# Kernel tuning notes

Hardware: AMD Instinct MI355X
Metric: run time of the kernel (lower is better)

The kernel has to match this reference:

```python
import jax, jax.numpy as jnp
import numpy as np

NUM_HEADS = 16
N_QUBITS = 8  # both attention d_k and FFN qubit count
LN_EPS = 1e-5


def setup_inputs() -> dict:
    key = jax.random.key(0)
    ks = jax.random.split(key, 8)
    B, S, E, F = 8, 4096, 128, 2048
    return {
        "x": jax.random.normal(ks[0], (B, S, E), dtype=jnp.float32),
        "theta_attn": jax.random.normal(ks[1], (N_QUBITS,), dtype=jnp.float32),
        "phi_ffn": jax.random.normal(ks[2], (N_QUBITS,), dtype=jnp.float32),
        "w1": jax.random.normal(ks[3], (F, N_QUBITS), dtype=jnp.float32) * (1.0 / np.sqrt(N_QUBITS)),
        "b1": jax.random.normal(ks[4], (F,), dtype=jnp.float32) * 0.01,
        "w2": jax.random.normal(ks[5], (E, F), dtype=jnp.float32) * (1.0 / np.sqrt(F)),
        "b2": jax.random.normal(ks[6], (E,), dtype=jnp.float32) * 0.01,
        "gamma1": jnp.ones((E,), dtype=jnp.float32),
        "beta1": jnp.zeros((E,), dtype=jnp.float32),
        "gamma2": jnp.ones((E,), dtype=jnp.float32),
        "beta2": jnp.zeros((E,), dtype=jnp.float32),
    }


def _layernorm(y, g, b):
    m = jnp.mean(y, axis=-1, keepdims=True)
    v = jnp.var(y, axis=-1, keepdims=True)
    return (y - m) * jax.lax.rsqrt(v + LN_EPS) * g + b


def _quantum_attn(x, theta):
    # RX(x_k)RX(theta_k) per wire -> per-wire <Z>=cos(x_k+theta_k); CNOT chain + ring
    # maps Z_j -> Z_0..Z_j (j>=1) and Z_0 -> Z_0..Z_{n-1} (Heisenberg picture),
    # so outputs are cumulative products of cosines within each head.
    B, S, E = x.shape
    a = x.reshape(B, S, NUM_HEADS, N_QUBITS) + theta  # (B,S,H,8)
    cp = jnp.cumprod(jnp.cos(a), axis=-1)
    out = jnp.concatenate([cp[..., -1:], cp[..., 1:]], axis=-1)  # wire0 gets full product
    return out.reshape(B, S, E)


def _quantum_ffn(x, phi):
    # RY(phi_j)RX(x_j)|0> -> <Z_j> = cos(phi_j)*cos(x_j); encoder only reads first N_QUBITS feats
    return jnp.cos(phi) * jnp.cos(x[..., :N_QUBITS])  # (B,S,8)


def reference(x, theta_attn, phi_ffn, w1, b1, w2, b2, gamma1, beta1, gamma2, beta2):
    attn = _quantum_attn(x, theta_attn)
    x1 = _layernorm(x + attn, gamma1, beta1)  # dropout is identity in eval
    q = _quantum_ffn(x1, phi_ffn)
    h = jax.nn.relu(jnp.einsum('bsq,fq->bsf', q, w1) + b1)
    ffn = jnp.einsum('bsf,ef->bse', h, w2) + b2
    return _layernorm(x1 + ffn, gamma2, beta2)
```

## Files before the change

kernel.cpp:

```cpp
#include <hip/hip_runtime.h>
#include <hip/hip_bf16.h>

typedef __attribute__((ext_vector_type(8))) short short8;
typedef __attribute__((ext_vector_type(4))) float f32x4;
typedef __attribute__((ext_vector_type(4))) int int4v;

#define LN_EPS 1e-5f

__device__ __forceinline__ unsigned short bf16rn(float f) {
    unsigned int u = __builtin_bit_cast(unsigned int, f);
    u = u + 0x7fffu + ((u >> 16) & 1u);
    return (unsigned short)(u >> 16);
}

__device__ __forceinline__ unsigned cvt_pk(float lo, float hi) {
    unsigned r;
    asm("v_cvt_pk_bf16_f32 %0, %1, %2" : "=v"(r) : "v"(lo), "v"(hi));
    return r;
}

__global__ __launch_bounds__(256) void k_prep(const float* __restrict__ w2,
                                              const float* __restrict__ w1,
                                              const float* __restrict__ b1,
                                              unsigned short* __restrict__ w2b,
                                              unsigned short* __restrict__ w1p) {
    const int bid = blockIdx.x;
    if (bid < 256) {
        int i = (bid * 256 + threadIdx.x) * 4;
        float4 v = *(const float4*)(w2 + i);
        ushort4 r;
        r.x = bf16rn(v.x); r.y = bf16rn(v.y); r.z = bf16rn(v.z); r.w = bf16rn(v.w);
        *(ushort4*)(w2b + i) = r;
    } else {
        int f = (bid - 256) * 256 + threadIdx.x;
        float4 wa = *(const float4*)(w1 + (size_t)f * 8);
        float4 wb = *(const float4*)(w1 + (size_t)f * 8 + 4);
        short8 r0, r1;
        r0[0] = (short)bf16rn(wa.x); r0[1] = (short)bf16rn(wa.y);
        r0[2] = (short)bf16rn(wa.z); r0[3] = (short)bf16rn(wa.w);
        r0[4] = (short)bf16rn(wb.x); r0[5] = (short)bf16rn(wb.y);
        r0[6] = (short)bf16rn(wb.z); r0[7] = (short)bf16rn(wb.w);
        r1 = short8{0, 0, 0, 0, 0, 0, 0, 0};
        r1[0] = (short)bf16rn(b1[f]);
        short8 z = short8{0, 0, 0, 0, 0, 0, 0, 0};
        unsigned short* row = w1p + (size_t)f * 32;
        *(short8*)(row) = r0;
        *(short8*)(row + 8) = r1;
        *(short8*)(row + 16) = z;
        *(short8*)(row + 24) = z;
    }
}

__global__ __launch_bounds__(256) void k_pre(const float* __restrict__ x,
                                             const float* __restrict__ theta,
                                             const float* __restrict__ phi,
                                             const float* __restrict__ gamma1,
                                             const float* __restrict__ beta1,
                                             float* __restrict__ x1,
                                             unsigned short* __restrict__ qpad) {
    const int tid = threadIdx.x;
    const int g = tid >> 4, li = tid & 15;
    const int tok = blockIdx.x * 16 + g;

    const float* xr = x + (size_t)tok * 128 + li * 8;
    float4 va = *(const float4*)xr;
    float4 vb = *(const float4*)(xr + 4);
    float v[8] = {va.x, va.y, va.z, va.w, vb.x, vb.y, vb.z, vb.w};

    float c[8];
#pragma unroll
    for (int k = 0; k < 8; ++k) c[k] = __cosf(v[k] + theta[k]);
    float cp[8];
    cp[0] = c[0];
#pragma unroll
    for (int k = 1; k < 8; ++k) cp[k] = cp[k - 1] * c[k];

    float y[8];
    y[0] = v[0] + cp[7];
#pragma unroll
    for (int k = 1; k < 8; ++k) y[k] = v[k] + cp[k];

    float s1 = 0.f, s2 = 0.f;
#pragma unroll
    for (int k = 0; k < 8; ++k) { s1 += y[k]; s2 += y[k] * y[k]; }
#pragma unroll
    for (int m = 1; m < 16; m <<= 1) {
        s1 += __shfl_xor(s1, m);
        s2 += __shfl_xor(s2, m);
    }
    float mean = s1 * (1.f / 128.f);
    float var = s2 * (1.f / 128.f) - mean * mean;
    float rs = rsqrtf(var + LN_EPS);

    float4 ga = *(const float4*)(gamma1 + li * 8);
    float4 gb = *(const float4*)(gamma1 + li * 8 + 4);
    float4 ba = *(const float4*)(beta1 + li * 8);
    float4 bb = *(const float4*)(beta1 + li * 8 + 4);
    float gam[8] = {ga.x, ga.y, ga.z, ga.w, gb.x, gb.y, gb.z, gb.w};
    float bet[8] = {ba.x, ba.y, ba.z, ba.w, bb.x, bb.y, bb.z, bb.w};

    float o[8];
#pragma unroll
    for (int k = 0; k < 8; ++k) o[k] = (y[k] - mean) * rs * gam[k] + bet[k];

    float* x1r = x1 + (size_t)tok * 128 + li * 8;
    *(float4*)x1r = make_float4(o[0], o[1], o[2], o[3]);
    *(float4*)(x1r + 4) = make_float4(o[4], o[5], o[6], o[7]);

    if (li == 0) {
        short8 qr;
#pragma unroll
        for (int k = 0; k < 8; ++k)
            qr[k] = (short)bf16rn(__cosf(phi[k]) * __cosf(o[k]));
        *(short8*)(qpad + (size_t)tok * 32) = qr;
    } else if (li < 4) {
        short8 z = short8{0, 0, 0, 0, 0, 0, 0, 0};
        if (li == 1) z[0] = (short)0x3F80;
        *(short8*)(qpad + (size_t)tok * 32 + li * 8) = z;
    }
}

__global__ __launch_bounds__(512) void k_ffn(const float* __restrict__ x1,
                                             const unsigned short* __restrict__ qpad,
                                             const unsigned short* __restrict__ w2b,
                                             const unsigned short* __restrict__ w1p,
                                             const float* __restrict__ b2,
                                             const float* __restrict__ g2,
                                             const float* __restrict__ be2,
                                             float* __restrict__ out) {
    const int tid = threadIdx.x;
    const int wv = tid >> 6;
    const int hf = wv >> 2;
    const int wvh = wv & 3;
    const int lane = tid & 63;
    const int li = lane & 15;
    const int lg = lane >> 4;
    const int Tb = blockIdx.x * 128;
    const int t0 = Tb + wvh * 32;

    __shared__ __align__(16) unsigned short Bs[2][2][128 * 64];
    __shared__ float red[128][132];

    short8 qf0 = *(const short8*)(qpad + (size_t)(t0 + li) * 32 + lg * 8);
    short8 qf1 = *(const short8*)(qpad + (size_t)(t0 + 16 + li) * 32 + lg * 8);

    const int arow0 = (8 * (li >> 2) + (li & 3)) * 32 + lg * 8;

    f32x4 acc0[8], acc1[8];
#pragma unroll
    for (int nt = 0; nt < 8; ++nt) {
        acc0[nt] = f32x4{0.f, 0.f, 0.f, 0.f};
        acc1[nt] = f32x4{0.f, 0.f, 0.f, 0.f};
    }

    const int srow = lane >> 3;
    const int scs = (lane & 7) ^ srow;

    auto stage = [&](int buf, int kb_local) {
        const int kb = hf * 1024 + kb_local;
#pragma unroll
        for (int r = 0; r < 4; ++r) {
            const int e0 = r * 32 + wvh * 8;
            const unsigned short* src =
                w2b + (size_t)(e0 + srow) * 2048 + kb + scs * 8;
            unsigned short* dst = &Bs[hf][buf][e0 * 64];
            __builtin_amdgcn_global_load_lds(
                (const __attribute__((address_space(1))) unsigned int*)src,
                (__attribute__((address_space(3))) unsigned int*)dst,
                16, 0, 0);
        }
    };

    stage(0, 0);
    __syncthreads();

    const f32x4 zero4 = f32x4{0.f, 0.f, 0.f, 0.f};

    for (int kbi = 0; kbi < 16; ++kbi) {
        const int buf = kbi & 1;
        if (kbi < 15) stage(buf ^ 1, (kbi + 1) * 64);

#pragma unroll
        for (int kk = 0; kk < 2; ++kk) {
            const int f = hf * 1024 + kbi * 64 + kk * 32;

            const unsigned short* wbase = w1p + (size_t)f * 32;
            short8 A0 = *(const short8*)(wbase + arow0);
            short8 A1 = *(const short8*)(wbase + arow0 + 128);

            const int cs = (kk * 4 + lg) ^ (li & 7);
            const unsigned short* basep = &Bs[hf][buf][li * 64 + cs * 8];
            short8 bfr[8];
#pragma unroll
            for (int nt = 0; nt < 8; ++nt)
                bfr[nt] = *(const short8*)(basep + nt * 1024);

            {
                f32x4 p0 = __builtin_amdgcn_mfma_f32_16x16x32_bf16(A0, qf0, zero4, 0, 0, 0);
                f32x4 p1 = __builtin_amdgcn_mfma_f32_16x16x32_bf16(A1, qf0, zero4, 0, 0, 0);
#pragma unroll
                for (int r = 0; r < 4; ++r) {
                    p0[r] = fmaxf(p0[r], 0.f);
                    p1[r] = fmaxf(p1[r], 0.f);
                }
                int4v ai = {(int)cvt_pk(p0[0], p0[1]), (int)cvt_pk(p0[2], p0[3]),
                            (int)cvt_pk(p1[0], p1[1]), (int)cvt_pk(p1[2], p1[3])};
                short8 a2 = __builtin_bit_cast(short8, ai);
#pragma unroll
                for (int nt = 0; nt < 8; ++nt)
                    acc0[nt] = __builtin_amdgcn_mfma_f32_16x16x32_bf16(a2, bfr[nt], acc0[nt], 0, 0, 0);
            }
            {
                f32x4 p0 = __builtin_amdgcn_mfma_f32_16x16x32_bf16(A0, qf1, zero4, 0, 0, 0);
                f32x4 p1 = __builtin_amdgcn_mfma_f32_16x16x32_bf16(A1, qf1, zero4, 0, 0, 0);
#pragma unroll
                for (int r = 0; r < 4; ++r) {
                    p0[r] = fmaxf(p0[r], 0.f);
                    p1[r] = fmaxf(p1[r], 0.f);
                }
                int4v ai = {(int)cvt_pk(p0[0], p0[1]), (int)cvt_pk(p0[2], p0[3]),
                            (int)cvt_pk(p1[0], p1[1]), (int)cvt_pk(p1[2], p1[3])};
                short8 a2 = __builtin_bit_cast(short8, ai);
#pragma unroll
                for (int nt = 0; nt < 8; ++nt)
                    acc1[nt] = __builtin_amdgcn_mfma_f32_16x16x32_bf16(a2, bfr[nt], acc1[nt], 0, 0, 0);
            }
        }
        __syncthreads();
    }

    if (hf == 1) {
#pragma unroll
        for (int mt = 0; mt < 2; ++mt) {
            const f32x4* acc = mt ? acc1 : acc0;
#pragma unroll
            for (int nt = 0; nt < 8; ++nt)
#pragma unroll
                for (int r = 0; r < 4; ++r)
                    red[wvh * 32 + mt * 16 + lg * 4 + r][nt * 16 + li] = acc[nt][r];
        }
    }
    __syncthreads();
    if (hf == 0) {
#pragma unroll
        for (int mt = 0; mt < 2; ++mt) {
            f32x4* acc = mt ? acc1 : acc0;
#pragma unroll
            for (int nt = 0; nt < 8; ++nt)
#pragma unroll
                for (int r = 0; r < 4; ++r)
                    acc[nt][r] += red[wvh * 32 + mt * 16 + lg * 4 + r][nt * 16 + li];
        }

        float b2v[8], g2v[8], be2v[8];
#pragma unroll
        for (int nt = 0; nt < 8; ++nt) {
            int e = nt * 16 + li;
            b2v[nt] = b2[e]; g2v[nt] = g2[e]; be2v[nt] = be2[e];
        }

        auto epilogue = [&](const f32x4(&acc)[8], int mt) {
#pragma unroll
            for (int r = 0; r < 4; ++r) {
                const int trow = t0 + mt * 16 + lg * 4 + r;
                const float* x1r = x1 + (size_t)trow * 128;
                float vals[8];
                float s1 = 0.f, s2 = 0.f;
#pragma unroll
                for (int nt = 0; nt < 8; ++nt) {
                    float vv = acc[nt][r] + b2v[nt] + x1r[nt * 16 + li];
                    vals[nt] = vv;
                    s1 += vv;
                    s2 += vv * vv;
                }
#pragma unroll
                for (int m = 1; m < 16; m <<= 1) {
                    s1 += __shfl_xor(s1, m);
                    s2 += __shfl_xor(s2, m);
                }
                float mean = s1 * (1.f / 128.f);
                float var = s2 * (1.f / 128.f) - mean * mean;
                float rs = rsqrtf(var + LN_EPS);
                float* orow = out + (size_t)trow * 128;
#pragma unroll
                for (int nt = 0; nt < 8; ++nt)
                    orow[nt * 16 + li] = (vals[nt] - mean) * rs * g2v[nt] + be2v[nt];
            }
        };
        epilogue(acc0, 0);
        epilogue(acc1, 1);
    }
}

extern "C" void kernel_launch(void* const* d_in, const int* in_sizes, int n_in,
                              void* d_out, int out_size, void* d_ws, size_t ws_size,
                              hipStream_t stream) {
    const float* x      = (const float*)d_in[0];
    const float* theta  = (const float*)d_in[1];
    const float* phi    = (const float*)d_in[2];
    const float* w1     = (const float*)d_in[3];
    const float* b1     = (const float*)d_in[4];
    const float* w2     = (const float*)d_in[5];
    const float* b2     = (const float*)d_in[6];
    const float* gamma1 = (const float*)d_in[7];
    const float* beta1  = (const float*)d_in[8];
    const float* gamma2 = (const float*)d_in[9];
    const float* beta2  = (const float*)d_in[10];
    float* out = (float*)d_out;

    char* ws = (char*)d_ws;
    unsigned short* w2b  = (unsigned short*)ws;
    unsigned short* w1p  = (unsigned short*)(ws + (512 << 10));
    unsigned short* qpad = (unsigned short*)(ws + (1 << 20));

    k_prep<<<264, 256, 0, stream>>>(w2, w1, b1, w2b, w1p);
    k_pre<<<2048, 256, 0, stream>>>(x, theta, phi, gamma1, beta1, out, qpad);
    k_ffn<<<256, 512, 0, stream>>>(out, qpad, w2b, w1p, b2, gamma2, beta2, out);
}
```

Measured before the change: 48.64 us.

## Retile FFN waves to 64 tokens by 64 columns to cut LDS B-fragment reads

Each wave now covers 64 tokens by 64 output columns instead of 32 tokens by 128 columns. Per k-step it reads 4 B fragments from LDS instead of 8, but recomputes the first-layer hidden MFMA 4 times instead of 2. Because LayerNorm now spans two waves, the epilogue needs a shared-memory partial-sum exchange and an extra barrier. The launch bounds also ask for 2 blocks per CU, which caps register use.

```diff
diff --git a/kernel.cpp b/kernel.cpp
--- a/kernel.cpp
+++ b/kernel.cpp
@@ -120,50 +120,55 @@
     }
 }
 
-__global__ __launch_bounds__(512) void k_ffn(const float* __restrict__ x1,
-                                             const unsigned short* __restrict__ qpad,
-                                             const unsigned short* __restrict__ w2b,
-                                             const unsigned short* __restrict__ w1p,
-                                             const float* __restrict__ b2,
-                                             const float* __restrict__ g2,
-                                             const float* __restrict__ be2,
-                                             float* __restrict__ out) {
+__global__ __launch_bounds__(512, 2) void k_ffn(const float* __restrict__ x1,
+                                                const unsigned short* __restrict__ qpad,
+                                                const unsigned short* __restrict__ w2b,
+                                                const unsigned short* __restrict__ w1p,
+                                                const float* __restrict__ b2,
+                                                const float* __restrict__ g2,
+                                                const float* __restrict__ be2,
+                                                float* __restrict__ out) {
     const int tid = threadIdx.x;
     const int wv = tid >> 6;
-    const int hf = wv >> 2;
-    const int wvh = wv & 3;
+    const int kh = wv >> 2;
+    const int sub = wv & 3;
+    const int nh = sub & 1;
+    const int mw = sub >> 1;
     const int lane = tid & 63;
     const int li = lane & 15;
     const int lg = lane >> 4;
     const int Tb = blockIdx.x * 128;
-    const int t0 = Tb + wvh * 32;
+    const int lt0 = mw * 64;
+    const int t0 = Tb + lt0;
 
     __shared__ __align__(16) unsigned short Bs[2][2][128 * 64];
     __shared__ float red[128][132];
-
-    short8 qf0 = *(const short8*)(qpad + (size_t)(t0 + li) * 32 + lg * 8);
-    short8 qf1 = *(const short8*)(qpad + (size_t)(t0 + 16 + li) * 32 + lg * 8);
+    __shared__ float sums[128][4];
+
+    short8 qf[4];
+#pragma unroll
+    for (int mt = 0; mt < 4; ++mt)
+        qf[mt] = *(const short8*)(qpad + (size_t)(t0 + mt * 16 + li) * 32 + lg * 8);
 
     const int arow0 = (8 * (li >> 2) + (li & 3)) * 32 + lg * 8;
 
-    f32x4 acc0[8], acc1[8];
-#pragma unroll
-    for (int nt = 0; nt < 8; ++nt) {
-        acc0[nt] = f32x4{0.f, 0.f, 0.f, 0.f};
-        acc1[nt] = f32x4{0.f, 0.f, 0.f, 0.f};
-    }
+    f32x4 acc[4][4];
+#pragma unroll
+    for (int mt = 0; mt < 4; ++mt)
+#pragma unroll
+        for (int nt = 0; nt < 4; ++nt) acc[mt][nt] = f32x4{0.f, 0.f, 0.f, 0.f};
 
     const int srow = lane >> 3;
     const int scs = (lane & 7) ^ srow;
 
     auto stage = [&](int buf, int kb_local) {
-        const int kb = hf * 1024 + kb_local;
+        const int kb = kh * 1024 + kb_local;
 #pragma unroll
         for (int r = 0; r < 4; ++r) {
-            const int e0 = r * 32 + wvh * 8;
+            const int e0 = r * 32 + sub * 8;
             const unsigned short* src =
                 w2b + (size_t)(e0 + srow) * 2048 + kb + scs * 8;
-            unsigned short* dst = &Bs[hf][buf][e0 * 64];
+            unsigned short* dst = &Bs[kh][buf][e0 * 64];
             __builtin_amdgcn_global_load_lds(
                 (const __attribute__((address_space(1))) unsigned int*)src,
                 (__attribute__((address_space(3))) unsigned int*)dst,
@@ -182,22 +187,23 @@
 
 #pragma unroll
         for (int kk = 0; kk < 2; ++kk) {
-            const int f = hf * 1024 + kbi * 64 + kk * 32;
+            const int f = kh * 1024 + kbi * 64 + kk * 32;
 
             const unsigned short* wbase = w1p + (size_t)f * 32;
             short8 A0 = *(const short8*)(wbase + arow0);
             short8 A1 = *(const short8*)(wbase + arow0 + 128);
 
             const int cs = (kk * 4 + lg) ^ (li & 7);
-            const unsigned short* basep = &Bs[hf][buf][li * 64 + cs * 8];
-            short8 bfr[8];
-#pragma unroll
-            for (int nt = 0; nt < 8; ++nt)
+            const unsigned short* basep = &Bs[kh][buf][(nh * 64 + li) * 64 + cs * 8];
+            short8 bfr[4];
+#pragma unroll
+            for (int nt = 0; nt < 4; ++nt)
                 bfr[nt] = *(const short8*)(basep + nt * 1024);
 
-            {
-                f32x4 p0 = __builtin_amdgcn_mfma_f32_16x16x32_bf16(A0, qf0, zero4, 0, 0, 0);
-                f32x4 p1 = __builtin_amdgcn_mfma_f32_16x16x32_bf16(A1, qf0, zero4, 0, 0, 0);
+#pragma unroll
+            for (int mt = 0; mt < 4; ++mt) {
+                f32x4 p0 = __builtin_amdgcn_mfma_f32_16x16x32_bf16(A0, qf[mt], zero4, 0, 0, 0);
+                f32x4 p1 = __builtin_amdgcn_mfma_f32_16x16x32_bf16(A1, qf[mt], zero4, 0, 0, 0);
 #pragma unroll
                 for (int r = 0; r < 4; ++r) {
                     p0[r] = fmaxf(p0[r], 0.f);
@@ -207,88 +213,78 @@
                             (int)cvt_pk(p1[0], p1[1]), (int)cvt_pk(p1[2], p1[3])};
                 short8 a2 = __builtin_bit_cast(short8, ai);
 #pragma unroll
-                for (int nt = 0; nt < 8; ++nt)
-                    acc0[nt] = __builtin_amdgcn_mfma_f32_16x16x32_bf16(a2, bfr[nt], acc0[nt], 0, 0, 0);
+                for (int nt = 0; nt < 4; ++nt)
+                    acc[mt][nt] = __builtin_amdgcn_mfma_f32_16x16x32_bf16(a2, bfr[nt], acc[mt][nt], 0, 0, 0);
             }
-            {
-                f32x4 p0 = __builtin_amdgcn_mfma_f32_16x16x32_bf16(A0, qf1, zero4, 0, 0, 0);
-                f32x4 p1 = __builtin_amdgcn_mfma_f32_16x16x32_bf16(A1, qf1, zero4, 0, 0, 0);
-#pragma unroll
-                for (int r = 0; r < 4; ++r) {
-                    p0[r] = fmaxf(p0[r], 0.f);
-                    p1[r] = fmaxf(p1[r], 0.f);
-                }
-                int4v ai = {(int)cvt_pk(p0[0], p0[1]), (int)cvt_pk(p0[2], p0[3]),
-                            (int)cvt_pk(p1[0], p1[1]), (int)cvt_pk(p1[2], p1[3])};
-                short8 a2 = __builtin_bit_cast(short8, ai);
-#pragma unroll
-                for (int nt = 0; nt < 8; ++nt)
-                    acc1[nt] = __builtin_amdgcn_mfma_f32_16x16x32_bf16(a2, bfr[nt], acc1[nt], 0, 0, 0);
-            }
         }
         __syncthreads();
     }
 
-    if (hf == 1) {
-#pragma unroll
-        for (int mt = 0; mt < 2; ++mt) {
-            const f32x4* acc = mt ? acc1 : acc0;
-#pragma unroll
-            for (int nt = 0; nt < 8; ++nt)
+    if (kh == 1) {
+#pragma unroll
+        for (int mt = 0; mt < 4; ++mt)
+#pragma unroll
+            for (int nt = 0; nt < 4; ++nt)
 #pragma unroll
                 for (int r = 0; r < 4; ++r)
-                    red[wvh * 32 + mt * 16 + lg * 4 + r][nt * 16 + li] = acc[nt][r];
-        }
+                    red[lt0 + mt * 16 + lg * 4 + r][nh * 64 + nt * 16 + li] = acc[mt][nt][r];
     }
     __syncthreads();
-    if (hf == 0) {
-#pragma unroll
-        for (int mt = 0; mt < 2; ++mt) {
-            f32x4* acc = mt ? acc1 : acc0;
-#pragma unroll
-            for (int nt = 0; nt < 8; ++nt)
-#pragma unroll
-                for (int r = 0; r < 4; ++r)
-                    acc[nt][r] += red[wvh * 32 + mt * 16 + lg * 4 + r][nt * 16 + li];
-        }
-
-        float b2v[8], g2v[8], be2v[8];
-#pragma unroll
-        for (int nt = 0; nt < 8; ++nt) {
-            int e = nt * 16 + li;
+
+    float b2v[4], g2v[4], be2v[4];
+    if (kh == 0) {
+#pragma unroll
+        for (int nt = 0; nt < 4; ++nt) {
+            int e = nh * 64 + nt * 16 + li;
             b2v[nt] = b2[e]; g2v[nt] = g2[e]; be2v[nt] = be2[e];
         }
-
-        auto epilogue = [&](const f32x4(&acc)[8], int mt) {
+#pragma unroll
+        for (int mt = 0; mt < 4; ++mt) {
 #pragma unroll
             for (int r = 0; r < 4; ++r) {
-                const int trow = t0 + mt * 16 + lg * 4 + r;
-                const float* x1r = x1 + (size_t)trow * 128;
-                float vals[8];
+                const int ltok = lt0 + mt * 16 + lg * 4 + r;
+                const int tok = Tb + ltok;
+                const float* x1r = x1 + (size_t)tok * 128 + nh * 64 + li;
                 float s1 = 0.f, s2 = 0.f;
 #pragma unroll
-                for (int nt = 0; nt < 8; ++nt) {
-                    float vv = acc[nt][r] + b2v[nt] + x1r[nt * 16 + li];
-                    vals[nt] = vv;
-                    s1 += vv;
-                    s2 += vv * vv;
+                for (int nt = 0; nt < 4; ++nt) {
+                    float v = acc[mt][nt][r] + red[ltok][nh * 64 + nt * 16 + li] +
+                              b2v[nt] + x1r[nt * 16];
+                    acc[mt][nt][r] = v;
+                    s1 += v; s2 += v * v;
                 }
 #pragma unroll
                 for (int m = 1; m < 16; m <<= 1) {
                     s1 += __shfl_xor(s1, m);
                     s2 += __shfl_xor(s2, m);
                 }
+                if (li == 0) {
+                    sums[ltok][nh * 2 + 0] = s1;
+                    sums[ltok][nh * 2 + 1] = s2;
+                }
+            }
+        }
+    }
+    __syncthreads();
+
+    if (kh == 0) {
+#pragma unroll
+        for (int mt = 0; mt < 4; ++mt) {
+#pragma unroll
+            for (int r = 0; r < 4; ++r) {
+                const int ltok = lt0 + mt * 16 + lg * 4 + r;
+                const int tok = Tb + ltok;
+                float s1 = sums[ltok][0] + sums[ltok][2];
+                float s2 = sums[ltok][1] + sums[ltok][3];
                 float mean = s1 * (1.f / 128.f);
                 float var = s2 * (1.f / 128.f) - mean * mean;
                 float rs = rsqrtf(var + LN_EPS);
-                float* orow = out + (size_t)trow * 128;
-#pragma unroll
-                for (int nt = 0; nt < 8; ++nt)
-                    orow[nt * 16 + li] = (vals[nt] - mean) * rs * g2v[nt] + be2v[nt];
+                float* orow = out + (size_t)tok * 128 + nh * 64 + li;
+#pragma unroll
+                for (int nt = 0; nt < 4; ++nt)
+                    orow[nt * 16] = (acc[mt][nt][r] - mean) * rs * g2v[nt] + be2v[nt];
             }
-        };
-        epilogue(acc0, 0);
-        epilogue(acc1, 1);
+        }
     }
 }
 
```

Result: slower. 55.79 us (+14.7%).
